# Kernel optimization log

Hardware: AMD Instinct MI355X
Metric: run time of the kernel (lower is better)

The kernel has to match this reference:

```python
import jax, jax.numpy as jnp
import numpy as np

DECAY = 0.99
EPS = 1e-05
DIM = 64
N_EMBED = 512
X_SHAPE = (32, 4096, DIM)


def setup_inputs() -> dict:
    key = jax.random.key(0)
    k1, k2 = jax.random.split(key)
    x = jax.random.normal(k1, X_SHAPE, dtype=jnp.float32)
    # codebook init uniform(-1/n_embed, 1/n_embed), as in torch .uniform_
    embed = jax.random.uniform(k2, (DIM, N_EMBED), dtype=jnp.float32,
                               minval=-1.0 / N_EMBED, maxval=1.0 / N_EMBED)
    cluster_size = jnp.zeros((N_EMBED,), dtype=jnp.float32)
    embed_avg = embed.copy()
    return {"x": x, "embed": embed, "cluster_size": cluster_size, "embed_avg": embed_avg}


def reference(x, embed, cluster_size, embed_avg):
    dim, n_embed = embed.shape
    flatten = x.reshape(-1, dim)  # [N, dim]
    # squared euclidean distance to each code: ||f||^2 - 2 f.E + ||E||^2  -> [N, n_embed]
    dist = (jnp.sum(flatten * flatten, axis=1, keepdims=True)
            - 2.0 * (flatten @ embed)
            + jnp.sum(embed * embed, axis=0, keepdims=True))
    embed_ind_flat = jnp.argmin(dist, axis=1)  # [N]
    embed_ind = embed_ind_flat.reshape(x.shape[:-1])
    quantize = jnp.take(embed.T, embed_ind_flat, axis=0).reshape(x.shape)

    # --- training-mode EMA buffer updates (no gradient flows; torch uses .data) ---
    f_sg = jax.lax.stop_gradient(flatten)
    # onehot.sum(0) == histogram of assignments; flatten.T @ onehot == segment_sum
    onehot_sum = jnp.zeros((n_embed,), dtype=x.dtype).at[embed_ind_flat].add(1.0)
    embed_sum = jax.ops.segment_sum(f_sg, embed_ind_flat, num_segments=n_embed).T  # [dim, n_embed]
    new_cluster_size = cluster_size * DECAY + (1.0 - DECAY) * onehot_sum
    new_embed_avg = embed_avg * DECAY + (1.0 - DECAY) * embed_sum
    n = jnp.sum(new_cluster_size)
    cs = (new_cluster_size + EPS) / (n + n_embed * EPS) * n
    new_embed = new_embed_avg / cs[None, :]

    diff = jnp.mean(jnp.square(jax.lax.stop_gradient(quantize) - x))
    quantize_st = x + jax.lax.stop_gradient(quantize - x)  # straight-through
    return quantize_st, diff, embed_ind, new_embed, new_cluster_size, new_embed_avg
```

## Files before the change

### kernel.cpp

```cpp
#include <hip/hip_runtime.h>

#define NVEC  131072
#define DIM   64
#define K     512
#define DECAYF 0.99f
#define OMDF   0.01f
#define EPSF   1e-5f
#define NBLK_ASSIGN (NVEC / 64)

#define Q_OFF    0
#define DIFF_OFF 8388608
#define IND_OFF  8388609
#define NE_OFF   8519681
#define NCS_OFF  8552449
#define NEA_OFF  8552961

#define ET_OFF    0
#define C_OFF     32768
#define DPART_OFF 33280
#define INDI_OFF  35328
#define PCNT_OFF  166400
#define PESUM_OFF 168448

__global__ __launch_bounds__(256) void vq_prep(const float* __restrict__ embed,
                                               float* __restrict__ ws) {
    #pragma clang fp contract(off)
    int j = blockIdx.x * 256 + threadIdx.x;
    float c = 0.0f;
    for (int d = 0; d < DIM; ++d) {
        float v = embed[d * K + j];
        ws[ET_OFF + j * DIM + d] = v;
        float t = v * v;
        c = c + t;
    }
    ws[C_OFF + j] = c;
}

__global__ __launch_bounds__(256)
__attribute__((amdgpu_waves_per_eu(4, 8)))
void vq_assign(
    const float* __restrict__ x,
    const float* __restrict__ ET,
    const float* __restrict__ C,
    int*   __restrict__ indI,
    float* __restrict__ dpart,
    float* __restrict__ out)
{
    #pragma clang fp contract(off)
    __shared__ float sd[4][64];
    __shared__ int   si[4][64];
    __shared__ int   sbest[64];
    __shared__ float wdl[4];

    int lane = threadIdx.x & 63;
    int wq   = __builtin_amdgcn_readfirstlane(threadIdx.x >> 6);
    int v    = blockIdx.x * 64 + lane;
    const float* fx = x + (size_t)v * DIM;

    float f[DIM];
    #pragma unroll
    for (int k = 0; k < DIM / 4; ++k) {
        float4 t = ((const float4*)fx)[k];
        f[4*k+0] = t.x; f[4*k+1] = t.y; f[4*k+2] = t.z; f[4*k+3] = t.w;
    }

    float r[8];
    #pragma unroll
    for (int k = 0; k < 8; ++k) r[k] = f[k] * f[k];
    #pragma unroll
    for (int b = 1; b < 8; ++b) {
        #pragma unroll
        for (int k = 0; k < 8; ++k) {
            float t = f[8*b + k] * f[8*b + k];
            r[k] = r[k] + t;
        }
    }
    float A = ((r[0] + r[1]) + (r[2] + r[3])) + ((r[4] + r[5]) + (r[6] + r[7]));

    const float* eseg = ET + (size_t)wq * 128 * DIM;
    const float* Cseg = C + wq * 128;
    float bestd = 3.0e38f;
    int   besti = wq * 128;
    #pragma unroll 4
    for (int jj = 0; jj < 128; ++jj) {
        const float* e = eseg + jj * DIM;
        float m = 0.0f;
        #pragma unroll
        for (int d = 0; d < DIM; ++d) m = __builtin_fmaf(f[d], e[d], m);
        float t1 = 2.0f * m;
        float t2 = A - t1;
        float dist = t2 + Cseg[jj];
        if (dist < bestd) { bestd = dist; besti = wq * 128 + jj; }
    }

    sd[wq][lane] = bestd;
    si[wq][lane] = besti;
    __syncthreads();

    if (wq == 0) {
        float bd = sd[0][lane];
        int   bi = si[0][lane];
        #pragma unroll
        for (int q = 1; q < 4; ++q) {
            float d2 = sd[q][lane];
            int   i2 = si[q][lane];
            if (d2 < bd || (d2 == bd && i2 < bi)) { bd = d2; bi = i2; }
        }
        sbest[lane] = bi;
        out[IND_OFF + v] = (float)bi;
        indI[v] = bi;
    }
    __syncthreads();

    int bi = sbest[lane];
    const float* qrow = ET + (size_t)bi * DIM + wq * 16;
    const float* xrow = fx + wq * 16;
    float* orow = out + Q_OFF + (size_t)v * DIM + wq * 16;
    float dl = 0.0f;
    #pragma unroll
    for (int k = 0; k < 4; ++k) {
        float4 tq = ((const float4*)qrow)[k];
        float4 tx = ((const float4*)xrow)[k];
        float r0 = tq.x - tx.x;
        float r1 = tq.y - tx.y;
        float r2 = tq.z - tx.z;
        float r3 = tq.w - tx.w;
        dl = __builtin_fmaf(r0, r0, dl); dl = __builtin_fmaf(r1, r1, dl);
        dl = __builtin_fmaf(r2, r2, dl); dl = __builtin_fmaf(r3, r3, dl);
        ((float4*)orow)[k] = tq;
    }

    #pragma unroll
    for (int off = 32; off > 0; off >>= 1) dl += __shfl_down(dl, off);
    if (lane == 0) wdl[wq] = dl;
    __syncthreads();
    if (threadIdx.x == 0)
        dpart[blockIdx.x] = ((wdl[0] + wdl[1]) + (wdl[2] + wdl[3]));
}

__global__ __launch_bounds__(512) void vq_stats(
    const float* __restrict__ x,
    const int* __restrict__ indI,
    float* __restrict__ pcnt,
    float* __restrict__ pesum)
{
    __shared__ float p[8][DIM];
    __shared__ float c[8];
    int j    = blockIdx.x >> 2;
    int q    = blockIdx.x & 3;
    int lane = threadIdx.x & 63;
    int w    = __builtin_amdgcn_readfirstlane(threadIdx.x >> 6);

    int seg  = q * 8 + w;
    int base = seg * (NVEC / 32);

    float acc = 0.0f;
    int   cnt = 0;
    for (int i = 0; i < NVEC / 32; i += 256) {
        int4 idv = ((const int4*)(indI + base + i))[lane];
        unsigned long long m0 = __ballot(idv.x == j);
        unsigned long long m1 = __ballot(idv.y == j);
        unsigned long long m2 = __ballot(idv.z == j);
        unsigned long long m3 = __ballot(idv.w == j);
        cnt += (int)(__popcll(m0) + __popcll(m1) + __popcll(m2) + __popcll(m3));
        while (m0) { int b = __builtin_ctzll(m0); m0 &= m0 - 1;
                     acc += x[(size_t)(base + i + 4*b + 0) * DIM + lane]; }
        while (m1) { int b = __builtin_ctzll(m1); m1 &= m1 - 1;
                     acc += x[(size_t)(base + i + 4*b + 1) * DIM + lane]; }
        while (m2) { int b = __builtin_ctzll(m2); m2 &= m2 - 1;
                     acc += x[(size_t)(base + i + 4*b + 2) * DIM + lane]; }
        while (m3) { int b = __builtin_ctzll(m3); m3 &= m3 - 1;
                     acc += x[(size_t)(base + i + 4*b + 3) * DIM + lane]; }
    }
    p[w][lane] = acc;
    if (lane == 0) c[w] = (float)cnt;
    __syncthreads();
    if (w == 0) {
        float s = ((p[0][lane] + p[1][lane]) + (p[2][lane] + p[3][lane]))
                + ((p[4][lane] + p[5][lane]) + (p[6][lane] + p[7][lane]));
        pesum[((size_t)q * K + j) * DIM + lane] = s;
        if (lane == 0)
            pcnt[q * K + j] = ((c[0] + c[1]) + (c[2] + c[3]))
                            + ((c[4] + c[5]) + (c[6] + c[7]));
    }
}

__global__ __launch_bounds__(512) void vq_finalize(
    const float* __restrict__ cluster_size,
    const float* __restrict__ embed_avg,
    const float* __restrict__ ws,
    float* __restrict__ out)
{
    __shared__ float wsum[8];
    __shared__ float dsum_sh[8];
    __shared__ float n_sh;
    int j = threadIdx.x;

    float cj = ((ws[PCNT_OFF + 0*K + j] + ws[PCNT_OFF + 1*K + j])
              + (ws[PCNT_OFF + 2*K + j] + ws[PCNT_OFF + 3*K + j]));
    float ncs = DECAYF * cluster_size[j] + OMDF * cj;
    out[NCS_OFF + j] = ncs;

    float dsum = 0.0f;
    #pragma unroll
    for (int k = 0; k < NBLK_ASSIGN / 512; ++k)
        dsum += ws[DPART_OFF + k * 512 + j];

    float s = ncs;
    #pragma unroll
    for (int off = 32; off > 0; off >>= 1) {
        s    += __shfl_down(s, off);
        dsum += __shfl_down(dsum, off);
    }
    if ((j & 63) == 0) { wsum[j >> 6] = s; dsum_sh[j >> 6] = dsum; }
    __syncthreads();
    if (j == 0) {
        float n = 0.f, dtot = 0.f;
        #pragma unroll
        for (int w = 0; w < 8; ++w) { n += wsum[w]; dtot += dsum_sh[w]; }
        n_sh = n;
        out[DIFF_OFF] = dtot * (1.0f / 8388608.0f);
    }
    __syncthreads();
    float n   = n_sh;
    float csz = (ncs + EPSF) / (n + (float)K * EPSF) * n;

    #pragma unroll 4
    for (int d = 0; d < DIM; ++d) {
        float es = ((ws[PESUM_OFF + ((size_t)0*K + j) * DIM + d]
                   + ws[PESUM_OFF + ((size_t)1*K + j) * DIM + d])
                  + (ws[PESUM_OFF + ((size_t)2*K + j) * DIM + d]
                   + ws[PESUM_OFF + ((size_t)3*K + j) * DIM + d]));
        float ea = DECAYF * embed_avg[d * K + j] + OMDF * es;
        out[NEA_OFF + d * K + j] = ea;
        out[NE_OFF  + d * K + j] = ea / csz;
    }
}

extern "C" void kernel_launch(void* const* d_in, const int* in_sizes, int n_in,
                              void* d_out, int out_size, void* d_ws, size_t ws_size,
                              hipStream_t stream) {
    const float* x            = (const float*)d_in[0];
    const float* embed        = (const float*)d_in[1];
    const float* cluster_size = (const float*)d_in[2];
    const float* embed_avg    = (const float*)d_in[3];
    float* out = (float*)d_out;
    float* ws  = (float*)d_ws;
    int*   indI = (int*)(ws + INDI_OFF);

    vq_prep<<<K / 256, 256, 0, stream>>>(embed, ws);
    vq_assign<<<NBLK_ASSIGN, 256, 0, stream>>>(
        x, ws + ET_OFF, ws + C_OFF, indI, ws + DPART_OFF, out);
    vq_stats<<<K * 4, 512, 0, stream>>>(
        x, indI, ws + PCNT_OFF, ws + PESUM_OFF);
    vq_finalize<<<1, K, 0, stream>>>(cluster_size, embed_avg, ws, out);
}
```

Measured before the change: 297.8 us.

## Split dot product across half-waves with pair-packed codebook and parallel finalize

The assign kernel now splits each vector's 64 dimensions across two half-waves. Each half-wave holds 32 features in registers and processes two codes per step from a new pair-interleaved codebook copy, passing partial sums between halves with a skewed cross-lane shuffle. This halves the per-thread register footprint and reuses each loaded feature for two codes, at the cost of extra shuffles and a one-step pipeline skew. The single-block finalize is also split: one kernel computes the normalised cluster sizes and a 64-block kernel writes the embed outputs from a transposed partial-sum layout, giving coalesced reads and more parallelism in exchange for one extra launch.

```diff
diff --git a/kernel.cpp b/kernel.cpp
--- a/kernel.cpp
+++ b/kernel.cpp
@@ -15,12 +15,14 @@
 #define NCS_OFF  8552449
 #define NEA_OFF  8552961
 
-#define ET_OFF    0
-#define C_OFF     32768
-#define DPART_OFF 33280
-#define INDI_OFF  35328
-#define PCNT_OFF  166400
-#define PESUM_OFF 168448
+#define ET_OFF     0
+#define C_OFF      32768
+#define EPK_OFF    33280
+#define CSZ_OFF    66048
+#define DPART_OFF  66560
+#define INDI_OFF   68608
+#define PCNT_OFF   199680
+#define PESUMT_OFF 201728
 
 __global__ __launch_bounds__(256) void vq_prep(const float* __restrict__ embed,
                                                float* __restrict__ ws) {
@@ -30,6 +32,7 @@
     for (int d = 0; d < DIM; ++d) {
         float v = embed[d * K + j];
         ws[ET_OFF + j * DIM + d] = v;
+        ws[EPK_OFF + (j >> 1) * (2 * DIM) + d * 2 + (j & 1)] = v;
         float t = v * v;
         c = c + t;
     }
@@ -37,85 +40,111 @@
 }
 
 __global__ __launch_bounds__(256)
-__attribute__((amdgpu_waves_per_eu(4, 8)))
+__attribute__((amdgpu_waves_per_eu(4, 4)))
 void vq_assign(
     const float* __restrict__ x,
     const float* __restrict__ ET,
-    const float* __restrict__ C,
+    const float2* __restrict__ EPK,
+    const float* __restrict__ Cn,
     int*   __restrict__ indI,
     float* __restrict__ dpart,
     float* __restrict__ out)
 {
     #pragma clang fp contract(off)
-    __shared__ float sd[4][64];
-    __shared__ int   si[4][64];
+    __shared__ float sd[2][64];
+    __shared__ int   si[2][64];
     __shared__ int   sbest[64];
     __shared__ float wdl[4];
 
-    int lane = threadIdx.x & 63;
-    int wq   = __builtin_amdgcn_readfirstlane(threadIdx.x >> 6);
-    int v    = blockIdx.x * 64 + lane;
-    const float* fx = x + (size_t)v * DIM;
-
-    float f[DIM];
-    #pragma unroll
-    for (int k = 0; k < DIM / 4; ++k) {
-        float4 t = ((const float4*)fx)[k];
-        f[4*k+0] = t.x; f[4*k+1] = t.y; f[4*k+2] = t.z; f[4*k+3] = t.w;
-    }
-
+    int t    = threadIdx.x;
+    int lane = t & 63;
+    int wav  = __builtin_amdgcn_readfirstlane(t >> 6);
+    int vg   = wav & 1;
+    int kp   = wav >> 1;
+    int vl   = lane & 31;
+    int h    = lane >> 5;
+    int vloc = vg * 32 + vl;
+    int v    = blockIdx.x * 64 + vloc;
+
+    const float* fx = x + (size_t)v * DIM + h * 32;
+    float f[32];
+    #pragma unroll
+    for (int k = 0; k < 8; ++k) {
+        float4 tt = ((const float4*)fx)[k];
+        f[4*k+0] = tt.x; f[4*k+1] = tt.y; f[4*k+2] = tt.z; f[4*k+3] = tt.w;
+    }
+
+    float p[8];
+    #pragma unroll
+    for (int k = 0; k < 8; ++k) p[k] = f[k] * f[k];
+    #pragma unroll
+    for (int b = 1; b < 4; ++b) {
+        #pragma unroll
+        for (int k = 0; k < 8; ++k) { float tq = f[8*b+k] * f[8*b+k]; p[k] = p[k] + tq; }
+    }
     float r[8];
     #pragma unroll
-    for (int k = 0; k < 8; ++k) r[k] = f[k] * f[k];
-    #pragma unroll
-    for (int b = 1; b < 8; ++b) {
-        #pragma unroll
-        for (int k = 0; k < 8; ++k) {
-            float t = f[8*b + k] * f[8*b + k];
-            r[k] = r[k] + t;
+    for (int k = 0; k < 8; ++k) r[k] = __shfl_xor(p[k], 32);
+    #pragma unroll
+    for (int b = 0; b < 4; ++b) {
+        #pragma unroll
+        for (int k = 0; k < 8; ++k) { float tq = f[8*b+k] * f[8*b+k]; r[k] = r[k] + tq; }
+    }
+    float A = ((r[0] + r[1]) + (r[2] + r[3])) + ((r[4] + r[5]) + (r[6] + r[7]));
+
+    int jbase = kp * 256;
+    const float2* ebase = EPK + (size_t)(jbase >> 1) * DIM + h * 32;
+    const float*  Cs    = Cn + jbase;
+
+    float2 m2 = make_float2(0.0f, 0.0f);
+    float bestd = 3.0e38f;
+    int   besti = jbase;
+    for (int s = 0; s <= 128; ++s) {
+        int jp0 = s < 128 ? s : 127;
+        int jp1 = s > 0 ? s - 1 : 0;
+        float rx = __shfl_xor(m2.x, 32);
+        float ry = __shfl_xor(m2.y, 32);
+        float2 m;
+        m.x = h ? rx : 0.0f;
+        m.y = h ? ry : 0.0f;
+        int jp = h ? jp1 : jp0;
+        const float2* ep = ebase + (size_t)jp * DIM;
+        #pragma unroll
+        for (int dd = 0; dd < 32; ++dd) {
+            float2 e2 = ep[dd];
+            m.x = __builtin_fmaf(f[dd], e2.x, m.x);
+            m.y = __builtin_fmaf(f[dd], e2.y, m.y);
         }
-    }
-    float A = ((r[0] + r[1]) + (r[2] + r[3])) + ((r[4] + r[5]) + (r[6] + r[7]));
-
-    const float* eseg = ET + (size_t)wq * 128 * DIM;
-    const float* Cseg = C + wq * 128;
-    float bestd = 3.0e38f;
-    int   besti = wq * 128;
-    #pragma unroll 4
-    for (int jj = 0; jj < 128; ++jj) {
-        const float* e = eseg + jj * DIM;
-        float m = 0.0f;
-        #pragma unroll
-        for (int d = 0; d < DIM; ++d) m = __builtin_fmaf(f[d], e[d], m);
-        float t1 = 2.0f * m;
-        float t2 = A - t1;
-        float dist = t2 + Cseg[jj];
-        if (dist < bestd) { bestd = dist; besti = wq * 128 + jj; }
-    }
-
-    sd[wq][lane] = bestd;
-    si[wq][lane] = besti;
-    __syncthreads();
-
-    if (wq == 0) {
-        float bd = sd[0][lane];
-        int   bi = si[0][lane];
-        #pragma unroll
-        for (int q = 1; q < 4; ++q) {
-            float d2 = sd[q][lane];
-            int   i2 = si[q][lane];
-            if (d2 < bd || (d2 == bd && i2 < bi)) { bd = d2; bi = i2; }
+        if (s) {
+            float c0 = Cs[2*jp1];
+            float c1 = Cs[2*jp1 + 1];
+            float d0 = __builtin_fmaf(-2.0f, m.x, A) + c0;
+            float d1 = __builtin_fmaf(-2.0f, m.y, A) + c1;
+            int j0 = jbase + 2*jp1;
+            if (d0 < bestd) { bestd = d0; besti = j0; }
+            if (d1 < bestd) { bestd = d1; besti = j0 + 1; }
         }
-        sbest[lane] = bi;
-        out[IND_OFF + v] = (float)bi;
-        indI[v] = bi;
+        m2 = m;
+    }
+
+    if (h == 1) { sd[kp][vloc] = bestd; si[kp][vloc] = besti; }
+    __syncthreads();
+
+    if (t < 64) {
+        float b0 = sd[0][t]; int i0 = si[0][t];
+        float b1 = sd[1][t]; int i1 = si[1][t];
+        int bi = (b1 < b0) ? i1 : i0;
+        sbest[t] = bi;
+        out[IND_OFF + blockIdx.x * 64 + t] = (float)bi;
+        indI[blockIdx.x * 64 + t] = bi;
     }
     __syncthreads();
 
     int bi = sbest[lane];
-    const float* qrow = ET + (size_t)bi * DIM + wq * 16;
-    const float* xrow = fx + wq * 16;
-    float* orow = out + Q_OFF + (size_t)v * DIM + wq * 16;
+    int v2 = blockIdx.x * 64 + lane;
+    const float* qrow = ET + (size_t)bi * DIM + wav * 16;
+    const float* xrow = x + (size_t)v2 * DIM + wav * 16;
+    float* orow = out + Q_OFF + (size_t)v2 * DIM + wav * 16;
     float dl = 0.0f;
     #pragma unroll
     for (int k = 0; k < 4; ++k) {
@@ -129,12 +158,11 @@
         dl = __builtin_fmaf(r2, r2, dl); dl = __builtin_fmaf(r3, r3, dl);
         ((float4*)orow)[k] = tq;
     }
-
     #pragma unroll
     for (int off = 32; off > 0; off >>= 1) dl += __shfl_down(dl, off);
-    if (lane == 0) wdl[wq] = dl;
-    __syncthreads();
-    if (threadIdx.x == 0)
+    if (lane == 0) wdl[wav] = dl;
+    __syncthreads();
+    if (t == 0)
         dpart[blockIdx.x] = ((wdl[0] + wdl[1]) + (wdl[2] + wdl[3]));
 }
 
@@ -142,7 +170,7 @@
     const float* __restrict__ x,
     const int* __restrict__ indI,
     float* __restrict__ pcnt,
-    float* __restrict__ pesum)
+    float* __restrict__ pesumT)
 {
     __shared__ float p[8][DIM];
     __shared__ float c[8];
@@ -178,17 +206,16 @@
     if (w == 0) {
         float s = ((p[0][lane] + p[1][lane]) + (p[2][lane] + p[3][lane]))
                 + ((p[4][lane] + p[5][lane]) + (p[6][lane] + p[7][lane]));
-        pesum[((size_t)q * K + j) * DIM + lane] = s;
+        pesumT[((size_t)q * DIM + lane) * K + j] = s;
         if (lane == 0)
             pcnt[q * K + j] = ((c[0] + c[1]) + (c[2] + c[3]))
                             + ((c[4] + c[5]) + (c[6] + c[7]));
     }
 }
 
-__global__ __launch_bounds__(512) void vq_finalize(
+__global__ __launch_bounds__(512) void vq_nf(
     const float* __restrict__ cluster_size,
-    const float* __restrict__ embed_avg,
-    const float* __restrict__ ws,
+    float* __restrict__ ws,
     float* __restrict__ out)
 {
     __shared__ float wsum[8];
@@ -222,19 +249,24 @@
         out[DIFF_OFF] = dtot * (1.0f / 8388608.0f);
     }
     __syncthreads();
-    float n   = n_sh;
-    float csz = (ncs + EPSF) / (n + (float)K * EPSF) * n;
-
-    #pragma unroll 4
-    for (int d = 0; d < DIM; ++d) {
-        float es = ((ws[PESUM_OFF + ((size_t)0*K + j) * DIM + d]
-                   + ws[PESUM_OFF + ((size_t)1*K + j) * DIM + d])
-                  + (ws[PESUM_OFF + ((size_t)2*K + j) * DIM + d]
-                   + ws[PESUM_OFF + ((size_t)3*K + j) * DIM + d]));
-        float ea = DECAYF * embed_avg[d * K + j] + OMDF * es;
-        out[NEA_OFF + d * K + j] = ea;
-        out[NE_OFF  + d * K + j] = ea / csz;
-    }
+    float n = n_sh;
+    ws[CSZ_OFF + j] = (ncs + EPSF) / (n + (float)K * EPSF) * n;
+}
+
+__global__ __launch_bounds__(512) void vq_emit(
+    const float* __restrict__ embed_avg,
+    const float* __restrict__ ws,
+    float* __restrict__ out)
+{
+    int d = blockIdx.x;
+    int j = threadIdx.x;
+    float es = ((ws[PESUMT_OFF + ((size_t)0*DIM + d) * K + j]
+               + ws[PESUMT_OFF + ((size_t)1*DIM + d) * K + j])
+              + (ws[PESUMT_OFF + ((size_t)2*DIM + d) * K + j]
+               + ws[PESUMT_OFF + ((size_t)3*DIM + d) * K + j]));
+    float ea = DECAYF * embed_avg[d * K + j] + OMDF * es;
+    out[NEA_OFF + d * K + j] = ea;
+    out[NE_OFF  + d * K + j] = ea / ws[CSZ_OFF + j];
 }
 
 extern "C" void kernel_launch(void* const* d_in, const int* in_sizes, int n_in,
@@ -250,8 +282,10 @@
 
     vq_prep<<<K / 256, 256, 0, stream>>>(embed, ws);
     vq_assign<<<NBLK_ASSIGN, 256, 0, stream>>>(
-        x, ws + ET_OFF, ws + C_OFF, indI, ws + DPART_OFF, out);
+        x, ws + ET_OFF, (const float2*)(ws + EPK_OFF), ws + C_OFF,
+        indI, ws + DPART_OFF, out);
     vq_stats<<<K * 4, 512, 0, stream>>>(
-        x, indI, ws + PCNT_OFF, ws + PESUM_OFF);
-    vq_finalize<<<1, K, 0, stream>>>(cluster_size, embed_avg, ws, out);
-}
+        x, indI, ws + PCNT_OFF, ws + PESUMT_OFF);
+    vq_nf<<<1, 512, 0, stream>>>(cluster_size, ws, out);
+    vq_emit<<<DIM, 512, 0, stream>>>(embed_avg, ws, out);
+}
```

Result: slower. 606.3 us (+103.6%).
